# Kernel tuning notes

Hardware: AMD Instinct MI355X
Metric: run time of the kernel (lower is better)

The kernel has to match this reference:

```python
import jax, jax.numpy as jnp
import numpy as np
from jax import lax

B, C, H, W = 8, 512, 64, 64
COUT, K = 512, 3
STYLE_DIM = 512


def setup_inputs() -> dict:
    key = jax.random.key(0)
    k1, k2, k3, k4, k5 = jax.random.split(key, 5)
    x = jax.random.normal(k1, (B, C, H, W), dtype=jnp.float32)
    style = jax.random.normal(k2, (B, STYLE_DIM), dtype=jnp.float32)
    # conv weight (OIHW), scaled like a typical init
    weight = jax.random.normal(k3, (COUT, C, K, K), dtype=jnp.float32) * (1.0 / np.sqrt(C * K * K))
    # modulation Linear: style_dim -> in_channels
    mod_w = jax.random.normal(k4, (C, STYLE_DIM), dtype=jnp.float32) * (1.0 / np.sqrt(STYLE_DIM))
    mod_b = jnp.ones((C,), dtype=jnp.float32) + 0.01 * jax.random.normal(k5, (C,), dtype=jnp.float32)
    return {"x": x, "style": style, "weight": weight, "mod_w": mod_w, "mod_b": mod_b}


def reference(x, style, weight, mod_w, mod_b):
    # s = modulation(style): Linear, shape (B, C) -> per-sample per-channel scale
    s = style @ mod_w.T + mod_b  # (B, C)
    xm = x * s[:, :, None, None]  # modulate input (B, C, H, W)
    # The torch code runs conv2d(groups=B) with weight.repeat(B,1,1,1); since the
    # weight is identical per group this equals a plain batched conv.
    y = lax.conv_general_dilated(
        xm, weight,
        window_strides=(1, 1),
        padding=[(1, 1), (1, 1)],
        rhs_dilation=(1, 1),
        dimension_numbers=("NCHW", "OIHW", "NCHW"),
    )  # (B, COUT, H, W)
    return y
```

## Files before the change

kernel.cpp:

```cpp
#include <hip/hip_runtime.h>
#include <cstdint>
#include <cstddef>

typedef short s16x8 __attribute__((ext_vector_type(8)));
typedef float f32x16 __attribute__((ext_vector_type(16)));

#define WS_S     0
#define WS_ZERO  16384
#define WS_XQ    32768
#define XQ_BYTES (8 * 64 * 64 * 64 * 16)
#define WS_WQ    (WS_XQ + XQ_BYTES)
#define WQ_BYTES (4 * 32 * 9 * 2 * 128 * 8 * 2)
#define WS_NEEDED ((size_t)WS_WQ + (size_t)WQ_BYTES)

__device__ __forceinline__ short f2bf(float f) {
  unsigned u = __builtin_bit_cast(unsigned, f);
  unsigned r = (u + 0x7fffu + ((u >> 16) & 1u)) >> 16;
  return (short)r;
}

__device__ __forceinline__ void gload_lds16(const void* g, void* l) {
  __builtin_amdgcn_global_load_lds(
      (const __attribute__((address_space(1))) void*)g,
      (__attribute__((address_space(3))) void*)l, 16, 0, 0);
}

__global__ void k_style(const float* __restrict__ style,
                        const float* __restrict__ mod_w,
                        const float* __restrict__ mod_b,
                        float* __restrict__ s_out,
                        float* __restrict__ zb) {
  if (blockIdx.x == 0) zb[threadIdx.x] = 0.0f;
  int wave = threadIdx.x >> 6, lane = threadIdx.x & 63;
  int wid = blockIdx.x * 4 + wave;
  int b = wid >> 9, c = wid & 511;
  const float4* st = (const float4*)(style + b * 512);
  const float4* mw = (const float4*)(mod_w + c * 512);
  float4 a0 = st[lane * 2], a1 = st[lane * 2 + 1];
  float4 b0 = mw[lane * 2], b1 = mw[lane * 2 + 1];
  float sum = a0.x * b0.x + a0.y * b0.y + a0.z * b0.z + a0.w * b0.w +
              a1.x * b1.x + a1.y * b1.y + a1.z * b1.z + a1.w * b1.w;
  #pragma unroll
  for (int off = 32; off; off >>= 1) sum += __shfl_down(sum, off);
  if (lane == 0) s_out[b * 512 + c] = sum + mod_b[c];
}

__global__ void k_xq(const float* __restrict__ x, const float* __restrict__ s,
                     char* __restrict__ xq) {
  int t = blockIdx.x * 256 + threadIdx.x;
  int w = t & 63, cg = (t >> 6) & 63, h = (t >> 12) & 63, b = t >> 18;
  const float* xp = x + (((b * 512 + cg * 8) * 64 + h) * 64 + w);
  const float* sp = s + b * 512 + cg * 8;
  s16x8 v;
  #pragma unroll
  for (int j = 0; j < 8; ++j) v[j] = f2bf(xp[j * 4096] * sp[j]);
  *(s16x8*)(xq + (size_t)t * 16) = v;
}

__global__ void k_wq(const float* __restrict__ wt, char* __restrict__ wq) {
  int tap = blockIdx.x, ch = blockIdx.y, nb = blockIdx.z;
  int kg = threadIdx.x >> 7, n = threadIdx.x & 127;
  const float* wp = wt + ((size_t)(nb * 128 + n) * 512 + ch * 16 + kg * 8) * 9 + tap;
  s16x8 v;
  #pragma unroll
  for (int j = 0; j < 8; ++j) v[j] = f2bf(wp[j * 9]);
  size_t idx = ((size_t)(nb * 32 + ch) * 9 + tap) * 256 + kg * 128 + n;
  *(s16x8*)(wq + idx * 16) = v;
}

__global__ __launch_bounds__(512, 2) void k_conv(
    const char* __restrict__ xq, const char* __restrict__ wq,
    const char* __restrict__ zerob, float* __restrict__ out) {
  extern __shared__ char smem[];
  char* wt_base = smem;
  char* xs_base = smem + 73728;

  const int tid = threadIdx.x;
  const int lane = tid & 63, wave = tid >> 6;
  const int l5 = lane >> 5, l31 = lane & 31;
  const int wc = wave >> 2;
  const int wp = wave & 3;
  const int mb = blockIdx.x, nb = blockIdx.y;
  const int b = mb >> 3;
  const int row0 = (mb & 7) << 3;

  if (tid < 80) {
    int dbuf = tid / 40, q = tid % 40;
    int j = q >> 2, kg = (q >> 1) & 1, side = q & 1;
    s16x8 z = {0, 0, 0, 0, 0, 0, 0, 0};
    *(s16x8*)(xs_base + dbuf * 21120 + ((j * 2 + kg) * 66 + side * 65) * 16) = z;
  }

  f32x16 acc[2][4];
  #pragma unroll
  for (int i = 0; i < 2; ++i)
    #pragma unroll
    for (int j = 0; j < 4; ++j)
      #pragma unroll
      for (int e = 0; e < 16; ++e) acc[i][j][e] = 0.0f;

  const char* wq_base = wq + (size_t)nb * (32 * 36864) + lane * 16;
  const char* xq_base = xq + (size_t)b * 4194304 + lane * 16;

  const int a_off = l5 * 2048 + l31 * 16;
  const int b_off = l5 * 1056 + l31 * 16;
  const int xs_woff = wp * 4224;

  #define STAGE(buf, ch)                                                      \
    _Pragma("unroll")                                                         \
    for (int i = 0; i < 7; ++i) {                                             \
      int seg = wave * 7 + i;                        \
      if (seg < 36) {                                                         \
        gload_lds16(wq_base + (size_t)(ch) * 36864 + seg * 1024,              \
                    wt_base + (buf) * 36864 + seg * 1024);                    \
      } else {                                                                \
        int q = seg - 36, j = q >> 1, kg = q & 1;                             \
        int h = row0 - 1 + j;                                                 \
        const char* src = (h >= 0 && h < 64)                                  \
            ? xq_base + (size_t)(h * 64 + (ch) * 2 + kg) * 1024               \
            : zerob + lane * 16;                                              \
        gload_lds16(src, xs_base + (buf) * 21120 + ((j * 2 + kg) * 66 + 1) * 16); \
      }                                                                       \
    }

  STAGE(0, 0);
  __syncthreads();

  for (int ch = 0; ch < 32; ++ch) {
    const int cur = ch & 1;
    if (ch < 31) STAGE(cur ^ 1, ch + 1);

    const char* wt = wt_base + cur * 36864;
    const char* xs_w = xs_base + cur * 21120 + xs_woff;

    #pragma unroll
    for (int kw = 0; kw < 3; ++kw) {
      s16x8 bC[4][2];
      #pragma unroll
      for (int r4 = 0; r4 < 4; ++r4)
        #pragma unroll
        for (int chh = 0; chh < 2; ++chh)
          bC[r4][chh] = *(const s16x8*)(xs_w + (r4 * 132 + chh * 32 + kw) * 16 + b_off);
      #pragma unroll
      for (int kh = 0; kh < 3; ++kh) {
        const int tap = kh * 3 + kw;
        s16x8 afr[2];
        #pragma unroll
        for (int ct = 0; ct < 2; ++ct)
          afr[ct] = *(const s16x8*)(wt + tap * 4096 + (wc * 2 + ct) * 512 + a_off);
        #pragma unroll
        for (int ct = 0; ct < 2; ++ct)
          #pragma unroll
          for (int pt = 0; pt < 4; ++pt)
            acc[ct][pt] = __builtin_amdgcn_mfma_f32_32x32x16_bf16(
                afr[ct], bC[(pt >> 1) + kh][pt & 1], acc[ct][pt], 0, 0, 0);
      }
    }
    __syncthreads();
  }

  #pragma unroll
  for (int ct = 0; ct < 2; ++ct) {
    #pragma unroll
    for (int pt = 0; pt < 4; ++pt) {
      int h = row0 + wp * 2 + (pt >> 1);
      int w = (pt & 1) * 32 + l31;
      int cb = nb * 128 + wc * 64 + ct * 32 + 4 * l5;
      #pragma unroll
      for (int rg = 0; rg < 16; ++rg) {
        int cout = cb + (rg & 3) + 8 * (rg >> 2);
        out[((size_t)(b * 512 + cout) * 4096) + h * 64 + w] = acc[ct][pt][rg];
      }
    }
  }
  #undef STAGE
}

__global__ void k_naive(const float* __restrict__ x, const float* __restrict__ style,
                        const float* __restrict__ wt, const float* __restrict__ mw,
                        const float* __restrict__ mb_, float* __restrict__ out) {
  __shared__ float s_sh[512];
  int h = blockIdx.x, co = blockIdx.y, b = blockIdx.z, w = threadIdx.x;
  for (int c = w; c < 512; c += 64) {
    float a = mb_[c];
    for (int k = 0; k < 512; ++k) a += style[b * 512 + k] * mw[c * 512 + k];
    s_sh[c] = a;
  }
  __syncthreads();
  float acc = 0.0f;
  for (int c = 0; c < 512; ++c) {
    float sc = s_sh[c];
    const float* wp = wt + ((size_t)co * 512 + c) * 9;
    for (int kh = 0; kh < 3; ++kh) {
      int hy = h + kh - 1;
      if (hy < 0 || hy >= 64) continue;
      for (int kw = 0; kw < 3; ++kw) {
        int wx = w + kw - 1;
        if (wx < 0 || wx >= 64) continue;
        acc += wp[kh * 3 + kw] * x[((size_t)(b * 512 + c) * 64 + hy) * 64 + wx] * sc;
      }
    }
  }
  out[((size_t)(b * 512 + co) * 64 + h) * 64 + w] = acc;
}

extern "C" void kernel_launch(void* const* d_in, const int* in_sizes, int n_in,
                              void* d_out, int out_size, void* d_ws, size_t ws_size,
                              hipStream_t stream) {
  const float* x      = (const float*)d_in[0];
  const float* style  = (const float*)d_in[1];
  const float* weight = (const float*)d_in[2];
  const float* mod_w  = (const float*)d_in[3];
  const float* mod_b  = (const float*)d_in[4];
  float* out = (float*)d_out;
  char* ws = (char*)d_ws;

  if (ws_size >= WS_NEEDED) {
    float* s  = (float*)(ws + WS_S);
    float* zb = (float*)(ws + WS_ZERO);
    char* xq  = ws + WS_XQ;
    char* wq  = ws + WS_WQ;
    k_style<<<1024, 256, 0, stream>>>(style, mod_w, mod_b, s, zb);
    k_xq<<<8192, 256, 0, stream>>>(x, s, xq);
    k_wq<<<dim3(9, 32, 4), 256, 0, stream>>>(weight, wq);
    k_conv<<<dim3(64, 4), 512, 115968, stream>>>(xq, wq, (const char*)zb, out);
  } else {
    k_naive<<<dim3(64, 512, 8), 64, 0, stream>>>(x, style, weight, mod_w, mod_b, out);
  }
}
```

Before: 154.0 us.

## Interleave next-chunk LDS staging across kw steps with barrier-bracketed MFMA phases

The single block of global-to-LDS loads for the next channel chunk is split into three parts, one issued inside each kw step. All A-fragment LDS reads for the step are hoisted ahead of its MFMA cluster. Each MFMA cluster is bracketed by s_barrier and raised wave priority (setprio), and the vmcnt wait happens only before the last step, so waves work in lockstep and memory traffic overlaps compute more evenly. The cost is six barriers per chunk instead of one, plus higher register use for the hoisted A fragments.

```diff
diff --git a/kernel.cpp b/kernel.cpp
--- a/kernel.cpp
+++ b/kernel.cpp
@@ -106,9 +106,9 @@
   const int b_off = l5 * 1056 + l31 * 16;
   const int xs_woff = wp * 4224;
 
-  #define STAGE(buf, ch)                                                      \
+  #define STAGE_PART(buf, ch, i0, i1)                                         \
     _Pragma("unroll")                                                         \
-    for (int i = 0; i < 7; ++i) {                                             \
+    for (int i = (i0); i < (i1); ++i) {                                       \
       int seg = wave * 7 + i;                        \
       if (seg < 36) {                                                         \
         gload_lds16(wq_base + (size_t)(ch) * 36864 + seg * 1024,              \
@@ -123,40 +123,53 @@
       }                                                                       \
     }
 
-  STAGE(0, 0);
-  __syncthreads();
+  STAGE_PART(0, 0, 0, 7);
+  asm volatile("s_waitcnt vmcnt(0) lgkmcnt(0)" ::: "memory");
+  __builtin_amdgcn_s_barrier();
 
   for (int ch = 0; ch < 32; ++ch) {
     const int cur = ch & 1;
-    if (ch < 31) STAGE(cur ^ 1, ch + 1);
-
     const char* wt = wt_base + cur * 36864;
     const char* xs_w = xs_base + cur * 21120 + xs_woff;
 
     #pragma unroll
     for (int kw = 0; kw < 3; ++kw) {
-      s16x8 bC[4][2];
+      s16x8 bC[4][2], aF[3][2];
       #pragma unroll
       for (int r4 = 0; r4 < 4; ++r4)
         #pragma unroll
         for (int chh = 0; chh < 2; ++chh)
           bC[r4][chh] = *(const s16x8*)(xs_w + (r4 * 132 + chh * 32 + kw) * 16 + b_off);
       #pragma unroll
-      for (int kh = 0; kh < 3; ++kh) {
-        const int tap = kh * 3 + kw;
-        s16x8 afr[2];
+      for (int kh = 0; kh < 3; ++kh)
         #pragma unroll
         for (int ct = 0; ct < 2; ++ct)
-          afr[ct] = *(const s16x8*)(wt + tap * 4096 + (wc * 2 + ct) * 512 + a_off);
+          aF[kh][ct] = *(const s16x8*)(wt + (kh * 3 + kw) * 4096 + (wc * 2 + ct) * 512 + a_off);
+
+      if (ch < 31) {
+        if (kw == 0)      STAGE_PART(cur ^ 1, ch + 1, 0, 3)
+        else if (kw == 1) STAGE_PART(cur ^ 1, ch + 1, 3, 5)
+        else              STAGE_PART(cur ^ 1, ch + 1, 5, 7)
+      }
+
+      __builtin_amdgcn_sched_barrier(0);
+      __builtin_amdgcn_s_barrier();
+
+      __builtin_amdgcn_s_setprio(1);
+      #pragma unroll
+      for (int kh = 0; kh < 3; ++kh)
         #pragma unroll
         for (int ct = 0; ct < 2; ++ct)
           #pragma unroll
           for (int pt = 0; pt < 4; ++pt)
             acc[ct][pt] = __builtin_amdgcn_mfma_f32_32x32x16_bf16(
-                afr[ct], bC[(pt >> 1) + kh][pt & 1], acc[ct][pt], 0, 0, 0);
-      }
-    }
-    __syncthreads();
+                aF[kh][ct], bC[(pt >> 1) + kh][pt & 1], acc[ct][pt], 0, 0, 0);
+      __builtin_amdgcn_s_setprio(0);
+
+      if (kw == 2)
+        asm volatile("s_waitcnt vmcnt(0)" ::: "memory");
+      __builtin_amdgcn_s_barrier();
+    }
   }
 
   #pragma unroll
@@ -173,7 +186,7 @@
       }
     }
   }
-  #undef STAGE
+  #undef STAGE_PART
 }
 
 __global__ void k_naive(const float* __restrict__ x, const float* __restrict__ style,
```

New measurement: 164.2 us. 6.6% more time.

## Hand-schedule LDS fragment reads with inline asm and prefetch across kw phases

Applied to the files above, without the earlier changes.

Replaces the compiler-scheduled LDS loads in the conv main loop with explicit ds_read_b128 inline asm using immediate offsets. A and B fragments are double-buffered in registers so the reads for the next kw phase are issued while the current phase's MFMAs run, with partial lgkmcnt waits and sched_barriers to pin the order. The MFMA clusters are also wrapped in s_setprio, and __syncthreads is replaced by an explicit vmcnt wait plus s_barrier. This raises register pressure and depends on hand-counted waitcnt values and offsets being correct.

```diff
diff --git a/kernel.cpp b/kernel.cpp
--- a/kernel.cpp
+++ b/kernel.cpp
@@ -102,9 +102,8 @@
   const char* wq_base = wq + (size_t)nb * (32 * 36864) + lane * 16;
   const char* xq_base = xq + (size_t)b * 4194304 + lane * 16;
 
-  const int a_off = l5 * 2048 + l31 * 16;
-  const int b_off = l5 * 1056 + l31 * 16;
-  const int xs_woff = wp * 4224;
+  const unsigned xs0 = (unsigned)(size_t)xs_base + wp * 4224 + l5 * 1056 + l31 * 16;
+  const unsigned wt0 = (unsigned)(size_t)wt_base + wc * 1024 + l5 * 2048 + l31 * 16;
 
   #define STAGE(buf, ch)                                                      \
     _Pragma("unroll")                                                         \
@@ -123,40 +122,73 @@
       }                                                                       \
     }
 
+  #define DSR(d, base, o) \
+    asm volatile("ds_read_b128 %0, %1 offset:" o : "=v"(d) : "v"(base))
+  #define SB() __builtin_amdgcn_sched_barrier(0)
+
+  #define MCL(aS, bS)                                                        \
+    __builtin_amdgcn_s_setprio(1);                                           \
+    _Pragma("unroll") for (int kh = 0; kh < 3; ++kh)                         \
+      _Pragma("unroll") for (int ct = 0; ct < 2; ++ct)                       \
+        _Pragma("unroll") for (int pt = 0; pt < 4; ++pt)                     \
+          acc[ct][pt] = __builtin_amdgcn_mfma_f32_32x32x16_bf16(             \
+              aS[kh][ct], bS[(pt >> 1) + kh][pt & 1], acc[ct][pt], 0, 0, 0); \
+    __builtin_amdgcn_s_setprio(0);
+
   STAGE(0, 0);
-  __syncthreads();
+  asm volatile("s_waitcnt vmcnt(0) lgkmcnt(0)" ::: "memory");
+  __builtin_amdgcn_s_barrier();
+
+  s16x8 aS0[3][2], bS0[4][2], aS1[3][2], bS1[4][2];
 
   for (int ch = 0; ch < 32; ++ch) {
     const int cur = ch & 1;
+    const unsigned bxs = xs0 + cur * 21120;
+    const unsigned bwt = wt0 + cur * 36864;
+
+    DSR(bS0[0][0], bxs, "0");     DSR(bS0[0][1], bxs, "512");
+    DSR(bS0[1][0], bxs, "2112");  DSR(bS0[1][1], bxs, "2624");
+    DSR(bS0[2][0], bxs, "4224");  DSR(bS0[2][1], bxs, "4736");
+    DSR(bS0[3][0], bxs, "6336");  DSR(bS0[3][1], bxs, "6848");
+    DSR(aS0[0][0], bwt, "0");     DSR(aS0[0][1], bwt, "512");
+    DSR(aS0[1][0], bwt, "12288"); DSR(aS0[1][1], bwt, "12800");
+    DSR(aS0[2][0], bwt, "24576"); DSR(aS0[2][1], bwt, "25088");
+    DSR(bS1[0][0], bxs, "16");    DSR(bS1[0][1], bxs, "528");
+    DSR(bS1[1][0], bxs, "2128");  DSR(bS1[1][1], bxs, "2640");
+    DSR(bS1[2][0], bxs, "4240");  DSR(bS1[2][1], bxs, "4752");
+    DSR(bS1[3][0], bxs, "6352");  DSR(bS1[3][1], bxs, "6864");
+
     if (ch < 31) STAGE(cur ^ 1, ch + 1);
 
-    const char* wt = wt_base + cur * 36864;
-    const char* xs_w = xs_base + cur * 21120 + xs_woff;
-
-    #pragma unroll
-    for (int kw = 0; kw < 3; ++kw) {
-      s16x8 bC[4][2];
-      #pragma unroll
-      for (int r4 = 0; r4 < 4; ++r4)
-        #pragma unroll
-        for (int chh = 0; chh < 2; ++chh)
-          bC[r4][chh] = *(const s16x8*)(xs_w + (r4 * 132 + chh * 32 + kw) * 16 + b_off);
-      #pragma unroll
-      for (int kh = 0; kh < 3; ++kh) {
-        const int tap = kh * 3 + kw;
-        s16x8 afr[2];
-        #pragma unroll
-        for (int ct = 0; ct < 2; ++ct)
-          afr[ct] = *(const s16x8*)(wt + tap * 4096 + (wc * 2 + ct) * 512 + a_off);
-        #pragma unroll
-        for (int ct = 0; ct < 2; ++ct)
-          #pragma unroll
-          for (int pt = 0; pt < 4; ++pt)
-            acc[ct][pt] = __builtin_amdgcn_mfma_f32_32x32x16_bf16(
-                afr[ct], bC[(pt >> 1) + kh][pt & 1], acc[ct][pt], 0, 0, 0);
-      }
-    }
-    __syncthreads();
+    asm volatile("s_waitcnt lgkmcnt(8)" ::: "memory");
+    SB();
+    MCL(aS0, bS0);
+    SB();
+
+    DSR(aS1[0][0], bwt, "4096");  DSR(aS1[0][1], bwt, "4608");
+    DSR(aS1[1][0], bwt, "16384"); DSR(aS1[1][1], bwt, "16896");
+    DSR(aS1[2][0], bwt, "28672"); DSR(aS1[2][1], bwt, "29184");
+    DSR(bS0[0][0], bxs, "32");    DSR(bS0[0][1], bxs, "544");
+    DSR(bS0[1][0], bxs, "2144");  DSR(bS0[1][1], bxs, "2656");
+    DSR(bS0[2][0], bxs, "4256");  DSR(bS0[2][1], bxs, "4768");
+    DSR(bS0[3][0], bxs, "6368");  DSR(bS0[3][1], bxs, "6880");
+
+    asm volatile("s_waitcnt lgkmcnt(8)" ::: "memory");
+    SB();
+    MCL(aS1, bS1);
+    SB();
+
+    DSR(aS0[0][0], bwt, "8192");  DSR(aS0[0][1], bwt, "8704");
+    DSR(aS0[1][0], bwt, "20480"); DSR(aS0[1][1], bwt, "20992");
+    DSR(aS0[2][0], bwt, "32768"); DSR(aS0[2][1], bwt, "33280");
+
+    asm volatile("s_waitcnt lgkmcnt(0)" ::: "memory");
+    SB();
+    MCL(aS0, bS0);
+    SB();
+
+    asm volatile("s_waitcnt vmcnt(0)" ::: "memory");
+    __builtin_amdgcn_s_barrier();
   }
 
   #pragma unroll
@@ -174,6 +206,9 @@
     }
   }
   #undef STAGE
+  #undef DSR
+  #undef SB
+  #undef MCL
 }
 
 __global__ void k_naive(const float* __restrict__ x, const float* __restrict__ style,
```

Result: slower. 169.1 us (+9.8%).

## Fuse input modulation and bf16 conversion into conv staging loop

Applied to the files above, without the earlier changes.

The separate k_xq pass is removed. The conv kernel now loads fp32 activations into registers for the next channel chunk, multiplies them by the style scale, packs them to bf16 and writes them to LDS after the MFMA work. The style and weight-prep kernels are merged into one launch, and MFMA blocks are wrapped in s_setprio. This drops a full write and reread of the bf16 activation tensor and two launches. In exchange the conv kernel carries more register pressure, and x is reread by each of the four output-channel blocks.

```diff
diff --git a/kernel.cpp b/kernel.cpp
--- a/kernel.cpp
+++ b/kernel.cpp
@@ -6,10 +6,7 @@
 typedef float f32x16 __attribute__((ext_vector_type(16)));
 
 #define WS_S     0
-#define WS_ZERO  16384
-#define WS_XQ    32768
-#define XQ_BYTES (8 * 64 * 64 * 64 * 16)
-#define WS_WQ    (WS_XQ + XQ_BYTES)
+#define WS_WQ    32768
 #define WQ_BYTES (4 * 32 * 9 * 2 * 128 * 8 * 2)
 #define WS_NEEDED ((size_t)WS_WQ + (size_t)WQ_BYTES)
 
@@ -25,52 +22,43 @@
       (__attribute__((address_space(3))) void*)l, 16, 0, 0);
 }
 
-__global__ void k_style(const float* __restrict__ style,
-                        const float* __restrict__ mod_w,
-                        const float* __restrict__ mod_b,
-                        float* __restrict__ s_out,
-                        float* __restrict__ zb) {
-  if (blockIdx.x == 0) zb[threadIdx.x] = 0.0f;
-  int wave = threadIdx.x >> 6, lane = threadIdx.x & 63;
-  int wid = blockIdx.x * 4 + wave;
-  int b = wid >> 9, c = wid & 511;
-  const float4* st = (const float4*)(style + b * 512);
-  const float4* mw = (const float4*)(mod_w + c * 512);
-  float4 a0 = st[lane * 2], a1 = st[lane * 2 + 1];
-  float4 b0 = mw[lane * 2], b1 = mw[lane * 2 + 1];
-  float sum = a0.x * b0.x + a0.y * b0.y + a0.z * b0.z + a0.w * b0.w +
-              a1.x * b1.x + a1.y * b1.y + a1.z * b1.z + a1.w * b1.w;
-  #pragma unroll
-  for (int off = 32; off; off >>= 1) sum += __shfl_down(sum, off);
-  if (lane == 0) s_out[b * 512 + c] = sum + mod_b[c];
-}
-
-__global__ void k_xq(const float* __restrict__ x, const float* __restrict__ s,
-                     char* __restrict__ xq) {
-  int t = blockIdx.x * 256 + threadIdx.x;
-  int w = t & 63, cg = (t >> 6) & 63, h = (t >> 12) & 63, b = t >> 18;
-  const float* xp = x + (((b * 512 + cg * 8) * 64 + h) * 64 + w);
-  const float* sp = s + b * 512 + cg * 8;
-  s16x8 v;
-  #pragma unroll
-  for (int j = 0; j < 8; ++j) v[j] = f2bf(xp[j * 4096] * sp[j]);
-  *(s16x8*)(xq + (size_t)t * 16) = v;
-}
-
-__global__ void k_wq(const float* __restrict__ wt, char* __restrict__ wq) {
-  int tap = blockIdx.x, ch = blockIdx.y, nb = blockIdx.z;
-  int kg = threadIdx.x >> 7, n = threadIdx.x & 127;
-  const float* wp = wt + ((size_t)(nb * 128 + n) * 512 + ch * 16 + kg * 8) * 9 + tap;
-  s16x8 v;
-  #pragma unroll
-  for (int j = 0; j < 8; ++j) v[j] = f2bf(wp[j * 9]);
-  size_t idx = ((size_t)(nb * 32 + ch) * 9 + tap) * 256 + kg * 128 + n;
-  *(s16x8*)(wq + idx * 16) = v;
+__global__ void k_prep(const float* __restrict__ style,
+                       const float* __restrict__ mod_w,
+                       const float* __restrict__ mod_b,
+                       const float* __restrict__ wt,
+                       float* __restrict__ s_out,
+                       char* __restrict__ wq) {
+  int bid = blockIdx.x;
+  if (bid < 1024) {
+    int wave = threadIdx.x >> 6, lane = threadIdx.x & 63;
+    int wid = bid * 4 + wave;
+    int b = wid >> 9, c = wid & 511;
+    const float4* st = (const float4*)(style + b * 512);
+    const float4* mw = (const float4*)(mod_w + c * 512);
+    float4 a0 = st[lane * 2], a1 = st[lane * 2 + 1];
+    float4 b0 = mw[lane * 2], b1 = mw[lane * 2 + 1];
+    float sum = a0.x * b0.x + a0.y * b0.y + a0.z * b0.z + a0.w * b0.w +
+                a1.x * b1.x + a1.y * b1.y + a1.z * b1.z + a1.w * b1.w;
+    #pragma unroll
+    for (int off = 32; off; off >>= 1) sum += __shfl_down(sum, off);
+    if (lane == 0) s_out[b * 512 + c] = sum + mod_b[c];
+  } else {
+    int q = bid - 1024;
+    int tap = q % 9, t2 = q / 9;
+    int ch = t2 % 32, nb = t2 / 32;
+    int kg = threadIdx.x >> 7, n = threadIdx.x & 127;
+    const float* wp = wt + ((size_t)(nb * 128 + n) * 512 + ch * 16 + kg * 8) * 9 + tap;
+    s16x8 v;
+    #pragma unroll
+    for (int j = 0; j < 8; ++j) v[j] = f2bf(wp[j * 9]);
+    size_t idx = ((size_t)(nb * 32 + ch) * 9 + tap) * 256 + kg * 128 + n;
+    *(s16x8*)(wq + idx * 16) = v;
+  }
 }
 
 __global__ __launch_bounds__(512, 2) void k_conv(
-    const char* __restrict__ xq, const char* __restrict__ wq,
-    const char* __restrict__ zerob, float* __restrict__ out) {
+    const float* __restrict__ x, const float* __restrict__ sbuf,
+    const char* __restrict__ wq, float* __restrict__ out) {
   extern __shared__ char smem[];
   char* wt_base = smem;
   char* xs_base = smem + 73728;
@@ -100,35 +88,72 @@
       for (int e = 0; e < 16; ++e) acc[i][j][e] = 0.0f;
 
   const char* wq_base = wq + (size_t)nb * (32 * 36864) + lane * 16;
-  const char* xq_base = xq + (size_t)b * 4194304 + lane * 16;
+  const float* sv = sbuf + b * 512;
 
   const int a_off = l5 * 2048 + l31 * 16;
   const int b_off = l5 * 1056 + l31 * 16;
   const int xs_woff = wp * 4224;
 
-  #define STAGE(buf, ch)                                                      \
+  #define STAGE_WT(buf, chv)                                                  \
     _Pragma("unroll")                                                         \
-    for (int i = 0; i < 7; ++i) {                                             \
-      int seg = wave * 7 + i;                        \
-      if (seg < 36) {                                                         \
-        gload_lds16(wq_base + (size_t)(ch) * 36864 + seg * 1024,              \
+    for (int i = 0; i < 5; ++i) {                                             \
+      int seg = wave * 5 + i;                                                 \
+      if (seg < 36)                                                           \
+        gload_lds16(wq_base + (size_t)(chv) * 36864 + seg * 1024,             \
                     wt_base + (buf) * 36864 + seg * 1024);                    \
-      } else {                                                                \
-        int q = seg - 36, j = q >> 1, kg = q & 1;                             \
+    }
+
+  float xr[3][8]; float sr[3][8];
+  #define XLOAD(chv)                                                          \
+    _Pragma("unroll")                                                         \
+    for (int it = 0; it < 3; ++it) {                                          \
+      int slot = tid + it * 512;                                              \
+      if (slot < 1280) {                                                      \
+        int j = slot >> 7, kg = (slot >> 6) & 1, col = slot & 63;             \
         int h = row0 - 1 + j;                                                 \
-        const char* src = (h >= 0 && h < 64)                                  \
-            ? xq_base + (size_t)(h * 64 + (ch) * 2 + kg) * 1024               \
-            : zerob + lane * 16;                                              \
-        gload_lds16(src, xs_base + (buf) * 21120 + ((j * 2 + kg) * 66 + 1) * 16); \
+        int c0 = (chv) * 16 + kg * 8;                                         \
+        if (h >= 0 && h < 64) {                                               \
+          const float* xp = x + ((size_t)(b * 512 + c0) << 12) + h * 64 + col;\
+          _Pragma("unroll")                                                   \
+          for (int jj = 0; jj < 8; ++jj) xr[it][jj] = xp[(size_t)jj << 12];   \
+          *(float4*)&sr[it][0] = *(const float4*)(sv + c0);                   \
+          *(float4*)&sr[it][4] = *(const float4*)(sv + c0 + 4);               \
+        }                                                                     \
       }                                                                       \
     }
 
-  STAGE(0, 0);
+  #define CWRITE(buf)                                                         \
+    _Pragma("unroll")                                                         \
+    for (int it = 0; it < 3; ++it) {                                          \
+      int slot = tid + it * 512;                                              \
+      if (slot < 1280) {                                                      \
+        int j = slot >> 7, kg = (slot >> 6) & 1, col = slot & 63;             \
+        int h = row0 - 1 + j;                                                 \
+        int4 iv = {0, 0, 0, 0};                                               \
+        if (h >= 0 && h < 64) {                                               \
+          unsigned pk0, pk1, pk2, pk3;                                        \
+          asm("v_cvt_pk_bf16_f32 %0, %1, %2" : "=v"(pk0)                      \
+              : "v"(xr[it][0] * sr[it][0]), "v"(xr[it][1] * sr[it][1]));      \
+          asm("v_cvt_pk_bf16_f32 %0, %1, %2" : "=v"(pk1)                      \
+              : "v"(xr[it][2] * sr[it][2]), "v"(xr[it][3] * sr[it][3]));      \
+          asm("v_cvt_pk_bf16_f32 %0, %1, %2" : "=v"(pk2)                      \
+              : "v"(xr[it][4] * sr[it][4]), "v"(xr[it][5] * sr[it][5]));      \
+          asm("v_cvt_pk_bf16_f32 %0, %1, %2" : "=v"(pk3)                      \
+              : "v"(xr[it][6] * sr[it][6]), "v"(xr[it][7] * sr[it][7]));      \
+          iv.x = (int)pk0; iv.y = (int)pk1; iv.z = (int)pk2; iv.w = (int)pk3; \
+        }                                                                     \
+        *(int4*)(xs_base + (buf) * 21120 + ((j * 2 + kg) * 66 + 1 + col) * 16) = iv; \
+      }                                                                       \
+    }
+
+  STAGE_WT(0, 0);
+  XLOAD(0);
+  CWRITE(0);
   __syncthreads();
 
   for (int ch = 0; ch < 32; ++ch) {
     const int cur = ch & 1;
-    if (ch < 31) STAGE(cur ^ 1, ch + 1);
+    if (ch < 31) { STAGE_WT(cur ^ 1, ch + 1); XLOAD(ch + 1); }
 
     const char* wt = wt_base + cur * 36864;
     const char* xs_w = xs_base + cur * 21120 + xs_woff;
@@ -148,14 +173,18 @@
         #pragma unroll
         for (int ct = 0; ct < 2; ++ct)
           afr[ct] = *(const s16x8*)(wt + tap * 4096 + (wc * 2 + ct) * 512 + a_off);
+        __builtin_amdgcn_s_setprio(1);
         #pragma unroll
         for (int ct = 0; ct < 2; ++ct)
           #pragma unroll
           for (int pt = 0; pt < 4; ++pt)
             acc[ct][pt] = __builtin_amdgcn_mfma_f32_32x32x16_bf16(
                 afr[ct], bC[(pt >> 1) + kh][pt & 1], acc[ct][pt], 0, 0, 0);
+        __builtin_amdgcn_s_setprio(0);
       }
     }
+
+    if (ch < 31) CWRITE(cur ^ 1);
     __syncthreads();
   }
 
@@ -173,7 +202,9 @@
       }
     }
   }
-  #undef STAGE
+  #undef STAGE_WT
+  #undef XLOAD
+  #undef CWRITE
 }
 
 __global__ void k_naive(const float* __restrict__ x, const float* __restrict__ style,
@@ -217,13 +248,9 @@
 
   if (ws_size >= WS_NEEDED) {
     float* s  = (float*)(ws + WS_S);
-    float* zb = (float*)(ws + WS_ZERO);
-    char* xq  = ws + WS_XQ;
     char* wq  = ws + WS_WQ;
-    k_style<<<1024, 256, 0, stream>>>(style, mod_w, mod_b, s, zb);
-    k_xq<<<8192, 256, 0, stream>>>(x, s, xq);
-    k_wq<<<dim3(9, 32, 4), 256, 0, stream>>>(weight, wq);
-    k_conv<<<dim3(64, 4), 512, 115968, stream>>>(xq, wq, (const char*)zb, out);
+    k_prep<<<2176, 256, 0, stream>>>(style, mod_w, mod_b, weight, s, wq);
+    k_conv<<<dim3(64, 4), 512, 115968, stream>>>(x, s, wq, out);
   } else {
     k_naive<<<dim3(64, 512, 8), 64, 0, stream>>>(x, style, weight, mod_w, mod_b, out);
   }
```

New measurement: 153.3 us. About the same (-0.4%).
